# Performance work log

Measured on AMD Instinct MI355X. Metric: run time of the kernel, lower is better.

The kernel has to match this reference:

```python
import jax, jax.numpy as jnp
import numpy as np

WIN = 4096   # win_size == nfft
HOP = 2048   # hop_size == win_size // 2 (COLA)


def _hann_periodic(n):
    # torch.hann_window default is periodic
    return (0.5 * (1.0 - jnp.cos(2.0 * jnp.pi * jnp.arange(n) / n))).astype(jnp.float32)


def _stft(x):
    # x: [B, L] real. Pad to multiple of HOP (as in get_stft_torch), then
    # frame with center=False, apply periodic Hann, one-sided rfft.
    L = x.shape[-1]
    pad = (-L) % HOP
    x = jnp.pad(x, ((0, 0), (0, pad)))
    Lp = L + pad
    T = 1 + (Lp - WIN) // HOP  # number of frames, static
    idx = jnp.arange(T)[:, None] * HOP + jnp.arange(WIN)[None, :]
    frames = x[:, idx] * _hann_periodic(WIN)
    S = jnp.fft.rfft(frames, axis=-1)
    return jnp.swapaxes(S, -1, -2)  # [B, F, T]


def _edr_db(S):
    # Energy decay relief: suffix sum of |S|^2 over time, in dB.
    # Replaces the original O(T^2) per-frame loop with a reverse cumsum.
    p = (S.real * S.real + S.imag * S.imag).astype(jnp.float32)  # [B, F, T]
    suffix = jnp.cumsum(p[..., ::-1], axis=-1)[..., ::-1]
    return 10.0 * jnp.log10(suffix)  # db(x, is_squared=True)


def setup_inputs() -> dict:
    key = jax.random.key(0)
    k1, k2 = jax.random.split(key)
    B, NFREQ = 32, 192000
    return {
        "target_response": jax.random.normal(k1, (B, NFREQ), dtype=jnp.float32),
        "achieved_response": jax.random.normal(k2, (B, NFREQ), dtype=jnp.float32),
    }


def reference(target_response, achieved_response):
    n = target_response.shape[-1]
    # torch.fft.irfft(x, n=x.shape[-1]) -> time-domain RIR of length n
    target_rir = jnp.fft.irfft(target_response, n=n).astype(jnp.float32)
    achieved_rir = jnp.fft.irfft(achieved_response, n=n).astype(jnp.float32)

    S_target = _stft(target_rir)   # [B, F, T] complex64
    S_ach = _stft(achieved_rir)

    target_edr = _edr_db(S_target)  # [B, F, T] float32
    ach_edr = _edr_db(S_ach)

    freq_loss = jnp.sum(jnp.abs(target_edr - ach_edr), axis=-1)  # [B, F]
    loss_per_item = jnp.sum(freq_loss, axis=-1) / jnp.sum(
        jnp.abs(target_edr), axis=(-2, -1)
    )  # [B]
    return jnp.sum(loss_per_item)
```

## Files before the change

### kernel.cpp

```cpp
#include <hip/hip_runtime.h>
#include <hip/hip_fp16.h>
#include <math.h>

#define NSIG 64
#define NROW 192000
#define NN   192000
#define LP   192512
#define NT   93
#define NF   2049
#define PSTR 2050
#define PTS  (NT*PSTR)
#define NK2  188
#define TWO_PI 6.28318530717958647692f
#define SQ2H  0.70710678118654752440f
#define DB_LOG2 3.01029995663981195f

#define WS_P_OFF   0
#define WS_A_OFF   24403200ULL
#define WS_Y_OFF   49044736ULL
#define WS_ACC_OFF 73686272ULL

__device__ __forceinline__ float2 cmul(float2 a, float2 b) {
    return make_float2(a.x*b.x - a.y*b.y, a.x*b.y + a.y*b.x);
}
__device__ __forceinline__ float2 cadd(float2 a, float2 b) {
    return make_float2(a.x + b.x, a.y + b.y);
}
__device__ __forceinline__ float2 csub(float2 a, float2 b) {
    return make_float2(a.x - b.x, a.y - b.y);
}
__device__ __forceinline__ float2 mul_nI(float2 z) { return make_float2(z.y, -z.x); }
__device__ __forceinline__ float2 mul_pI(float2 z) { return make_float2(-z.y, z.x); }
__device__ __forceinline__ __half2 f2h(float2 v) { return __float22half2_rn(v); }
__device__ __forceinline__ float2 h2f(__half2 h) { return __half22float2(h); }

__device__ __forceinline__ void dft8(float2 (&x)[8]) {
    float2 e0 = cadd(x[0], x[4]), e1 = csub(x[0], x[4]);
    float2 e2 = cadd(x[2], x[6]), e3 = csub(x[2], x[6]);
    float2 E0 = cadd(e0, e2), E2 = csub(e0, e2);
    float2 E1 = cadd(e1, mul_nI(e3)), E3 = csub(e1, mul_nI(e3));
    float2 o0 = cadd(x[1], x[5]), o1 = csub(x[1], x[5]);
    float2 o2 = cadd(x[3], x[7]), o3 = csub(x[3], x[7]);
    float2 O0 = cadd(o0, o2), O2 = csub(o0, o2);
    float2 O1 = cadd(o1, mul_nI(o3)), O3 = csub(o1, mul_nI(o3));
    float2 W1 = make_float2(SQ2H*(O1.x + O1.y), SQ2H*(O1.y - O1.x));
    float2 W2 = mul_nI(O2);
    float2 W3 = make_float2(SQ2H*(O3.y - O3.x), -SQ2H*(O3.x + O3.y));
    x[0] = cadd(E0, O0); x[4] = csub(E0, O0);
    x[1] = cadd(E1, W1); x[5] = csub(E1, W1);
    x[2] = cadd(E2, W2); x[6] = csub(E2, W2);
    x[3] = cadd(E3, W3); x[7] = csub(E3, W3);
}

__device__ __forceinline__ void dft8i(float2 (&x)[8]) {
    float2 e0 = cadd(x[0], x[4]), e1 = csub(x[0], x[4]);
    float2 e2 = cadd(x[2], x[6]), e3 = csub(x[2], x[6]);
    float2 E0 = cadd(e0, e2), E2 = csub(e0, e2);
    float2 E1 = cadd(e1, mul_pI(e3)), E3 = csub(e1, mul_pI(e3));
    float2 o0 = cadd(x[1], x[5]), o1 = csub(x[1], x[5]);
    float2 o2 = cadd(x[3], x[7]), o3 = csub(x[3], x[7]);
    float2 O0 = cadd(o0, o2), O2 = csub(o0, o2);
    float2 O1 = cadd(o1, mul_pI(o3)), O3 = csub(o1, mul_pI(o3));
    float2 W1 = make_float2(SQ2H*(O1.x - O1.y), SQ2H*(O1.x + O1.y));
    float2 W2 = mul_pI(O2);
    float2 W3 = make_float2(-SQ2H*(O3.x + O3.y), SQ2H*(O3.x - O3.y));
    x[0] = cadd(E0, O0); x[4] = csub(E0, O0);
    x[1] = cadd(E1, W1); x[5] = csub(E1, W1);
    x[2] = cadd(E2, W2); x[6] = csub(E2, W2);
    x[3] = cadd(E3, W3); x[7] = csub(E3, W3);
}

#define S3C 0.86602540378443865f
__device__ __forceinline__ void dft3i(float2& x0, float2& x1, float2& x2) {
    float2 u = cadd(x1, x2), v = csub(x1, x2);
    float2 w = make_float2(x0.x - 0.5f*u.x, x0.y - 0.5f*u.y);
    x0 = cadd(x0, u);
    float2 iv = make_float2(-S3C * v.y, S3C * v.x);
    x1 = cadd(w, iv);
    x2 = csub(w, iv);
}

#define C51 0.30901699437494742f
#define S51 0.95105651629515357f
#define C52 (-0.80901699437494742f)
#define S52 0.58778525229247313f
__device__ __forceinline__ void dft5i(float2& x0, float2& x1, float2& x2,
                                      float2& x3, float2& x4) {
    float2 t1 = cadd(x1, x4), t2 = csub(x1, x4);
    float2 t3 = cadd(x2, x3), t4 = csub(x2, x3);
    float2 s0 = x0;
    x0 = make_float2(s0.x + t1.x + t3.x, s0.y + t1.y + t3.y);
    float2 A1 = make_float2(s0.x + C51*t1.x + C52*t3.x, s0.y + C51*t1.y + C52*t3.y);
    float2 B1 = make_float2(S51*t2.x + S52*t4.x, S51*t2.y + S52*t4.y);
    float2 A2 = make_float2(s0.x + C52*t1.x + C51*t3.x, s0.y + C52*t1.y + C51*t3.y);
    float2 B2 = make_float2(S52*t2.x - S51*t4.x, S52*t2.y - S51*t4.y);
    x1 = make_float2(A1.x - B1.y, A1.y + B1.x);
    x4 = make_float2(A1.x + B1.y, A1.y - B1.x);
    x2 = make_float2(A2.x - B2.y, A2.y + B2.x);
    x3 = make_float2(A2.x + B2.y, A2.y - B2.x);
}

#define SSTR 520
__global__ void __launch_bounds__(256) k_stage1(const float* __restrict__ X0,
                                                const float* __restrict__ X1,
                                                __half2* __restrict__ A) {
    const int bid  = blockIdx.x;
    const int sig  = bid & 63;
    const int kb   = bid >> 6;
    const int base = kb * 16;
    const float* X = (sig < 32) ? (X0 + (size_t)sig * NROW)
                                : (X1 + (size_t)(sig - 32) * NROW);
    __shared__ float SR[8 * SSTR], SI[8 * SSTR];
    const int tid = threadIdx.x;
    const int row = tid & 7;
    const int ln  = tid >> 3;

    const int k2e0 = base + 2 * row;
    const int k2e  = (k2e0 < NK2) ? k2e0 : (NK2 - 1);
    const int k2o  = (k2e0 + 1 < NK2) ? (k2e0 + 1) : (NK2 - 1);

    #pragma unroll
    for (int m = 0; m < 16; ++m) {
        int i = ln + 32 * m;
        int ide = 375 * i + k2e;
        int ido = 375 * i + k2o;
        float xe = X[(ide <= 96000) ? ide : (NN - ide)];
        float xo = X[(ido <= 96000) ? ido : (NN - ido)];
        SR[SSTR * row + i] = xe;
        SI[SSTR * row + i] = xo;
    }
    __syncthreads();

    const int w = tid >> 6;
    const int l = tid & 63;
    float* sra = SR + SSTR * (2 * w);     float* sia = SI + SSTR * (2 * w);
    float* srb = SR + SSTR * (2 * w + 1); float* sib = SI + SSTR * (2 * w + 1);
    float2 xa[8], xb[8];

    #pragma unroll
    for (int n1 = 0; n1 < 8; ++n1) {
        int ad = l + 64 * n1;
        xa[n1] = make_float2(sra[ad], sia[ad]);
        xb[n1] = make_float2(srb[ad], sib[ad]);
    }
    dft8i(xa); dft8i(xb);
    {
        float sn, cs; __sincosf(TWO_PI * (float)l * (1.0f / 512.0f), &sn, &cs);
        float2 bw = make_float2(cs, sn), tw = bw;
        xa[1] = cmul(xa[1], tw); xb[1] = cmul(xb[1], tw);
        #pragma unroll
        for (int k = 2; k < 8; ++k) {
            tw = cmul(tw, bw);
            xa[k] = cmul(xa[k], tw); xb[k] = cmul(xb[k], tw);
        }
    }
    #pragma unroll
    for (int a2 = 0; a2 < 8; ++a2) {
        int ad = 64 * a2 + (l ^ (8 * a2));
        sra[ad] = xa[a2].x; sia[ad] = xa[a2].y;
        srb[ad] = xb[a2].x; sib[ad] = xb[a2].y;
    }
    __builtin_amdgcn_wave_barrier();

    const int l0 = l & 7, aa = l >> 3;
    #pragma unroll
    for (int l1 = 0; l1 < 8; ++l1) {
        int ad = 64 * aa + ((l0 + 8 * l1) ^ (8 * aa));
        xa[l1] = make_float2(sra[ad], sia[ad]);
        xb[l1] = make_float2(srb[ad], sib[ad]);
    }
    dft8i(xa); dft8i(xb);
    {
        float sn, cs; __sincosf(TWO_PI * (float)l0 * (1.0f / 64.0f), &sn, &cs);
        float2 bw = make_float2(cs, sn), tw = bw;
        xa[1] = cmul(xa[1], tw); xb[1] = cmul(xb[1], tw);
        #pragma unroll
        for (int k = 2; k < 8; ++k) {
            tw = cmul(tw, bw);
            xa[k] = cmul(xa[k], tw); xb[k] = cmul(xb[k], tw);
        }
    }
    #pragma unroll
    for (int b2 = 0; b2 < 8; ++b2) {
        int ad = 64 * b2 + 8 * aa + (l0 ^ b2);
        sra[ad] = xa[b2].x; sia[ad] = xa[b2].y;
        srb[ad] = xb[b2].x; sib[ad] = xb[b2].y;
    }
    __builtin_amdgcn_wave_barrier();

    const int a3 = l & 7, b3 = l >> 3;
    #pragma unroll
    for (int l0r = 0; l0r < 8; ++l0r) {
        int ad = 64 * b3 + 8 * a3 + (l0r ^ b3);
        xa[l0r] = make_float2(sra[ad], sia[ad]);
        xb[l0r] = make_float2(srb[ad], sib[ad]);
    }
    dft8i(xa); dft8i(xb);
    #pragma unroll
    for (int c = 0; c < 8; ++c) {
        int ad = a3 + 8 * b3 + 64 * c;
        sra[ad] = xa[c].x; sia[ad] = xa[c].y;
        srb[ad] = xb[c].x; sib[ad] = xb[c].y;
    }
    __syncthreads();

    if (k2e0 < NK2) {
        float sn, cs;
        __sincosf(TWO_PI * (float)(k2e * ln) * (1.0f / 192000.0f), &sn, &cs);
        float2 wke = make_float2(cs, sn);
        __sincosf(TWO_PI * (float)(32 * k2e) * (1.0f / 192000.0f), &sn, &cs);
        float2 ste = make_float2(cs, sn);
        __sincosf(TWO_PI * (float)(k2o * ln) * (1.0f / 192000.0f), &sn, &cs);
        float2 wko = make_float2(cs, sn);
        __sincosf(TWO_PI * (float)(32 * k2o) * (1.0f / 192000.0f), &sn, &cs);
        float2 sto = make_float2(cs, sn);
        const bool odd_ok = (k2e0 + 1 < NK2);
        __half2* Ae = A + ((size_t)sig * NK2 + k2e) * 512;
        __half2* Ao = A + ((size_t)sig * NK2 + k2o) * 512;
        const float* zr = SR + SSTR * row;
        const float* zi = SI + SSTR * row;
        #pragma unroll
        for (int m = 0; m < 16; ++m) {
            int k  = ln + 32 * m;
            int km = (512 - k) & 511;
            float2 Z  = make_float2(zr[k],  zi[k]);
            float2 Zm = make_float2(zr[km], zi[km]);
            float2 S = make_float2(Z.x + Zm.x, Z.y - Zm.y);
            float2 D = make_float2(Z.x - Zm.x, Z.y + Zm.y);
            float2 Xe = make_float2(0.5f * S.x, 0.5f * S.y);
            float2 Xo = make_float2(0.5f * D.y, -0.5f * D.x);
            Ae[k] = f2h(cmul(Xe, wke));
            if (odd_ok) Ao[k] = f2h(cmul(Xo, wko));
            wke = cmul(wke, ste);
            wko = cmul(wko, sto);
        }
    }
}

#define TP2 16
#define T1STR 17
__global__ void __launch_bounds__(256) k_stage2(const __half2* __restrict__ A,
                                                __half* __restrict__ Y) {
    const int t1b = blockIdx.x * (2 * TP2);
    const int sig = blockIdx.y;
    __shared__ float SRT[375 * T1STR], SIT[375 * T1STR];
    const int tid = threadIdx.x;

    if (blockIdx.x == 0) {
        for (int j = tid; j < 512; j += 256)
            Y[(size_t)sig * LP + NN + j] = __float2half(0.f);
    }

    for (int w = tid; w < 25 * TP2; w += 256) {
        int c = w >> 4, pl = w & 15;
        float2 v[15];
        const float2* Asf = (const float2*)(A + (size_t)sig * (NK2 * 512) + t1b + 2 * pl);
        #pragma unroll
        for (int a = 0; a < 15; ++a) {
            int k2 = 25 * a + c;
            if (k2 < NK2) {
                float2 raw = Asf[(size_t)k2 * 256];
                float2 fa = h2f(((const __half2*)&raw)[0]);
                float2 fb = h2f(((const __half2*)&raw)[1]);
                v[a] = make_float2(fa.x - fb.y, fa.y + fb.x);
            } else {
                float2 raw = Asf[(size_t)(375 - k2) * 256];
                float2 fa = h2f(((const __half2*)&raw)[0]);
                float2 fb = h2f(((const __half2*)&raw)[1]);
                v[a] = make_float2(fa.x + fb.y, fb.x - fa.y);
            }
        }
        #pragma unroll
        for (int r = 0; r < 5; ++r) dft3i(v[r], v[r + 5], v[r + 10]);
        float2 tw[15];
        tw[0] = make_float2(1.f, 0.f);
        float sn, cs; __sincosf(TWO_PI * (float)c * (1.0f / 375.0f), &sn, &cs);
        float2 stp = make_float2(cs, sn);
        #pragma unroll
        for (int e = 1; e < 15; ++e) tw[e] = cmul(tw[e - 1], stp);
        #pragma unroll
        for (int e3 = 0; e3 < 3; ++e3) {
            float2 h0 = v[5 * e3], h1, h2, h3, h4;
            if (e3 == 0) { h1 = v[1]; h2 = v[2]; h3 = v[3]; h4 = v[4]; }
            else if (e3 == 1) {
                h1 = cmul(v[6],  make_float2(0.91354545764260090f, 0.40673664307580021f));
                h2 = cmul(v[7],  make_float2(0.66913060635885821f, 0.74314482547739424f));
                h3 = cmul(v[8],  make_float2(0.30901699437494742f, 0.95105651629515357f));
                h4 = cmul(v[9],  make_float2(-0.10452846326765347f, 0.99452189536827334f));
            } else {
                h1 = cmul(v[11], make_float2(0.66913060635885821f, 0.74314482547739424f));
                h2 = cmul(v[12], make_float2(-0.10452846326765347f, 0.99452189536827334f));
                h3 = cmul(v[13], make_float2(-0.80901699437494742f, 0.58778525229247313f));
                h4 = cmul(v[14], make_float2(-0.97814760073380564f, -0.20791169081775934f));
            }
            dft5i(h0, h1, h2, h3, h4);
            float2 o0 = cmul(h0, tw[e3]);
            float2 o1 = cmul(h1, tw[e3 + 3]);
            float2 o2 = cmul(h2, tw[e3 + 6]);
            float2 o3 = cmul(h3, tw[e3 + 9]);
            float2 o4 = cmul(h4, tw[e3 + 12]);
            int r0 = ((e3     ) * 25 + c) * T1STR + pl;
            int r1 = ((e3 + 3 ) * 25 + c) * T1STR + pl;
            int r2 = ((e3 + 6 ) * 25 + c) * T1STR + pl;
            int r3 = ((e3 + 9 ) * 25 + c) * T1STR + pl;
            int r4 = ((e3 + 12) * 25 + c) * T1STR + pl;
            SRT[r0] = o0.x; SIT[r0] = o0.y;
            SRT[r1] = o1.x; SIT[r1] = o1.y;
            SRT[r2] = o2.x; SIT[r2] = o2.y;
            SRT[r3] = o3.x; SIT[r3] = o3.y;
            SRT[r4] = o4.x; SIT[r4] = o4.y;
        }
    }
    __syncthreads();

    if (tid < 15 * TP2) {
        int e = tid >> 4, pl = tid & 15;
        float2 t[25];
        #pragma unroll
        for (int c = 0; c < 25; ++c) {
            int rr = (e * 25 + c) * T1STR + pl;
            t[c] = make_float2(SRT[rr], SIT[rr]);
        }
        #pragma unroll
        for (int c2 = 0; c2 < 5; ++c2)
            dft5i(t[c2], t[c2 + 5], t[c2 + 10], t[c2 + 15], t[c2 + 20]);
        t[6]  = cmul(t[6],  make_float2(0.96858316112863108f, 0.24868988716485479f));
        t[11] = cmul(t[11], make_float2(0.87630668004386358f, 0.48175367410171532f));
        t[16] = cmul(t[16], make_float2(0.72896862742141155f, 0.68454710592868873f));
        t[21] = cmul(t[21], make_float2(0.53582679497899666f, 0.84432792550201508f));
        t[7]  = cmul(t[7],  make_float2(0.87630668004386358f, 0.48175367410171532f));
        t[12] = cmul(t[12], make_float2(0.53582679497899666f, 0.84432792550201508f));
        t[17] = cmul(t[17], make_float2(0.06279051952931337f, 0.99802672842827156f));
        t[22] = cmul(t[22], make_float2(-0.42577929156507272f, 0.90482705246601958f));
        t[8]  = cmul(t[8],  make_float2(0.72896862742141155f, 0.68454710592868873f));
        t[13] = cmul(t[13], make_float2(0.06279051952931337f, 0.99802672842827156f));
        t[18] = cmul(t[18], make_float2(-0.63742398974868975f, 0.77051324277578925f));
        t[23] = cmul(t[23], make_float2(-0.99211470131447788f, 0.12533323356430426f));
        t[9]  = cmul(t[9],  make_float2(0.53582679497899666f, 0.84432792550201508f));
        t[14] = cmul(t[14], make_float2(-0.42577929156507272f, 0.90482705246601958f));
        t[19] = cmul(t[19], make_float2(-0.99211470131447788f, 0.12533323356430426f));
        t[24] = cmul(t[24], make_float2(-0.63742398974868997f, -0.77051324277578903f));
        #pragma unroll
        for (int u5 = 0; u5 < 5; ++u5)
            dft5i(t[5*u5], t[5*u5 + 1], t[5*u5 + 2], t[5*u5 + 3], t[5*u5 + 4]);
        __half2* yb2 = (__half2*)(Y + (size_t)sig * LP + t1b + 2 * pl);
        #pragma unroll
        for (int u5 = 0; u5 < 5; ++u5)
            #pragma unroll
            for (int u5p = 0; u5p < 5; ++u5p) {
                int d = u5 + 5 * u5p;
                float2 wv = t[5 * u5 + u5p];
                yb2[(size_t)256 * (15 * d + e)] =
                    __floats2half2_rn(wv.x * (1.0f / 192000.0f),
                                      wv.y * (1.0f / 192000.0f));
            }
    }
}

__global__ void __launch_bounds__(256) k_stft(const __half* __restrict__ Y,
                                              __half* __restrict__ P,
                                              float* __restrict__ ACC) {
    const int bid = blockIdx.x;
    const int sig = bid & 63;
    const int fr  = bid >> 6;
    const int lt  = threadIdx.x;
    __shared__ float SR[2560], SI[2560];
    __shared__ float2 wt2[32];
    float2 x[8];
    float2 base2048;

    if (bid == 0 && lt < 64) ACC[lt] = 0.f;

    {
        const __half2* yb = (const __half2*)(Y + (size_t)sig * LP + (size_t)fr * 2048);
        float sn, cs;
        __sincosf(TWO_PI * (float)lt * (1.0f / 2048.0f), &sn, &cs);
        base2048 = make_float2(cs, sn);
        float2 ce = base2048;
        const float2 d1 = make_float2(0.99999882345170188f,
                                      0.00153398018628477f);
        float2 co = cmul(ce, d1);
        const float2 r45 = make_float2(SQ2H, SQ2H);
        #pragma unroll
        for (int r = 0; r < 8; ++r) {
            float2 v = h2f(yb[lt + 256 * r]);
            float we = 0.5f - 0.5f * ce.x;
            float wo = 0.5f - 0.5f * co.x;
            x[r] = make_float2(v.x * we, v.y * wo);
            ce = cmul(ce, r45);
            co = cmul(co, r45);
        }
    }
    dft8(x);
    {
        float2 b = make_float2(base2048.x, -base2048.y), tw = b;
        x[1] = cmul(x[1], tw);
        #pragma unroll
        for (int k = 2; k < 8; ++k) { tw = cmul(tw, b); x[k] = cmul(x[k], tw); }
    }
    #pragma unroll
    for (int k = 0; k < 8; ++k) { SR[k * 256 + lt] = x[k].x; SI[k * 256 + lt] = x[k].y; }
    if (lt < 32) {
        float sn, cs; __sincosf(-TWO_PI * (float)lt * (1.0f / 256.0f), &sn, &cs);
        wt2[lt] = make_float2(cs, sn);
    }
    __syncthreads();

    {
        const int k2 = lt >> 5, m1 = lt & 31;
        #pragma unroll
        for (int r = 0; r < 8; ++r) {
            int idx = k2 * 256 + m1 + 32 * r;
            x[r] = make_float2(SR[idx], SI[idx]);
        }
        dft8(x);
        float2 b = wt2[m1], tw = b;
        x[1] = cmul(x[1], tw);
        #pragma unroll
        for (int k = 2; k < 8; ++k) { tw = cmul(tw, b); x[k] = cmul(x[k], tw); }
        __syncthreads();
        #pragma unroll
        for (int j = 0; j < 8; ++j) {
            int idx = k2 * 288 + j * 36 + m1;
            SR[idx] = x[j].x; SI[idx] = x[j].y;
        }
    }
    __syncthreads();

    {
        const int k2 = lt >> 5, j2 = (lt >> 2) & 7, p1 = lt & 3;
        #pragma unroll
        for (int r = 0; r < 8; ++r) {
            int idx = k2 * 288 + j2 * 36 + p1 + 4 * r;
            x[r] = make_float2(SR[idx], SI[idx]);
        }
        dft8(x);
        float2 b = (p1 == 0) ? make_float2(1.f, 0.f)
                 : (p1 == 1) ? make_float2(0.98078528040323044f, -0.19509032201612827f)
                 : (p1 == 2) ? make_float2(0.92387953251128676f, -0.38268343236508977f)
                 :             make_float2(0.83146961230254524f, -0.55557023301960222f);
        float2 tw = b;
        x[1] = cmul(x[1], tw);
        #pragma unroll
        for (int k = 2; k < 8; ++k) { tw = cmul(tw, b); x[k] = cmul(x[k], tw); }
        __syncthreads();
        #pragma unroll
        for (int q = 0; q < 8; ++q) {
            int idx = 5 * (q * 64 + k2 * 8 + j2) + p1;
            SR[idx] = x[q].x; SI[idx] = x[q].y;
        }
    }
    __syncthreads();

    {
        float2 za[4], zb[4];
        #pragma unroll
        for (int p = 0; p < 4; ++p) {
            int ia = 5 * lt + p;
            za[p] = make_float2(SR[ia], SI[ia]);
            zb[p] = make_float2(SR[ia + 1280], SI[ia + 1280]);
        }
        __syncthreads();
        const int q2a = lt >> 6, k2 = (lt >> 3) & 7, j2 = lt & 7;
        const int kbase = k2 + 8 * j2;
        {
            float2 s0 = cadd(za[0], za[2]), s1 = csub(za[0], za[2]);
            float2 s2 = cadd(za[1], za[3]), s3 = csub(za[1], za[3]);
            float2 X0 = cadd(s0, s2), X2 = csub(s0, s2);
            float2 X1 = cadd(s1, mul_nI(s3)), X3 = csub(s1, mul_nI(s3));
            int ka = kbase + 64 * q2a;
            SR[ka]        = X0.x; SI[ka]        = X0.y;
            SR[ka + 512]  = X1.x; SI[ka + 512]  = X1.y;
            SR[ka + 1024] = X2.x; SI[ka + 1024] = X2.y;
            SR[ka + 1536] = X3.x; SI[ka + 1536] = X3.y;
        }
        {
            float2 s0 = cadd(zb[0], zb[2]), s1 = csub(zb[0], zb[2]);
            float2 s2 = cadd(zb[1], zb[3]), s3 = csub(zb[1], zb[3]);
            float2 X0 = cadd(s0, s2), X2 = csub(s0, s2);
            float2 X1 = cadd(s1, mul_nI(s3)), X3 = csub(s1, mul_nI(s3));
            int kb = kbase + 64 * (q2a + 4);
            SR[kb]        = X0.x; SI[kb]        = X0.y;
            SR[kb + 512]  = X1.x; SI[kb + 512]  = X1.y;
            SR[kb + 1024] = X2.x; SI[kb + 1024] = X2.y;
            SR[kb + 1536] = X3.x; SI[kb + 1536] = X3.y;
        }
    }
    __syncthreads();

    {
        __half* pb = P + (size_t)sig * PTS + (size_t)fr * PSTR;
        float c2 = sqrtf(0.5f * (1.f + base2048.x));
        float s2 = sqrtf(0.5f * (1.f - base2048.x));
        float2 wk = make_float2(c2, -s2);
        const float2 stp = make_float2(0.92387953251128676f,
                                       -0.38268343236508977f);
        #pragma unroll
        for (int j = 0; j < 8; ++j) {
            int k  = lt + 256 * j;
            int kc = (2048 - k) & 2047;
            float zr = SR[k],  zi = SI[k];
            float cr = SR[kc], ci = SI[kc];
            float Ex = 0.5f * (zr + cr), Ey = 0.5f * (zi - ci);
            float Ox = 0.5f * (zi + ci), Oy = -0.5f * (zr - cr);
            float Xx = Ex + wk.x * Ox - wk.y * Oy;
            float Xy = Ey + wk.x * Oy + wk.y * Ox;
            pb[k] = __float2half_rn(sqrtf(Xx * Xx + Xy * Xy));
            wk = cmul(wk, stp);
        }
        if (lt == 0) { float d0 = SR[0] - SI[0]; pb[2048] = __float2half_rn(fabsf(d0)); }
    }
}

__global__ void __launch_bounds__(256) k_edr(const __half* __restrict__ P,
                                             float* __restrict__ ACC) {
    const int b = blockIdx.y;
    const int f = blockIdx.x * 256 + threadIdx.x;
    const bool act = (f < NF);
    const __half* Pt = P + (size_t)b * PTS;
    const __half* Pa = P + (size_t)(b + 32) * PTS;
    float st = 0.f, sa = 0.f, num = 0.f, den = 0.f;
    if (act) {
        for (int t = NT - 1; t >= 0; --t) {
            float vt = __half2float(Pt[(size_t)t * PSTR + f]);
            float va = __half2float(Pa[(size_t)t * PSTR + f]);
            st += vt * vt;
            sa += va * va;
            float et = DB_LOG2 * __log2f(st);
            float ea = DB_LOG2 * __log2f(sa);
            num += fabsf(et - ea);
            den += fabsf(et);
        }
    }
    for (int off = 32; off > 0; off >>= 1) {
        num += __shfl_down(num, off);
        den += __shfl_down(den, off);
    }
    __shared__ float sn_[4], sd_[4];
    int wave = threadIdx.x >> 6, lane = threadIdx.x & 63;
    if (lane == 0) { sn_[wave] = num; sd_[wave] = den; }
    __syncthreads();
    if (threadIdx.x == 0) {
        float n = sn_[0] + sn_[1] + sn_[2] + sn_[3];
        float d = sd_[0] + sd_[1] + sd_[2] + sd_[3];
        atomicAdd(&ACC[2 * b], n);
        atomicAdd(&ACC[2 * b + 1], d);
    }
}

__global__ void k_final(const float* __restrict__ ACC, float* __restrict__ out) {
    int tid = threadIdx.x;
    float r = 0.f;
    if (tid < 32) r = ACC[2 * tid] / ACC[2 * tid + 1];
    for (int off = 32; off > 0; off >>= 1) r += __shfl_down(r, off);
    if (tid == 0) out[0] = r;
}

extern "C" void kernel_launch(void* const* d_in, const int* in_sizes, int n_in,
                              void* d_out, int out_size, void* d_ws, size_t ws_size,
                              hipStream_t stream) {
    const float* X0 = (const float*)d_in[0];
    const float* X1 = (const float*)d_in[1];
    float* out = (float*)d_out;

    char* base = (char*)d_ws;
    __half*  P  = (__half*)(base + WS_P_OFF);
    __half2* A  = (__half2*)(base + WS_A_OFF);
    __half*  Y  = (__half*)(base + WS_Y_OFF);
    float*   ACC = (float*)(base + WS_ACC_OFF);

    k_stage1<<<dim3(768),      dim3(256), 0, stream>>>(X0, X1, A);
    k_stage2<<<dim3(16, 64),   dim3(256), 0, stream>>>(A, Y);
    k_stft  <<<dim3(5952),     dim3(256), 0, stream>>>(Y, P, ACC);
    k_edr   <<<dim3(9, 32),    dim3(256), 0, stream>>>(P, ACC);
    k_final <<<1, 64, 0, stream>>>(ACC, out);
}
```

Before: 79.20 us.

## Give each wave one FFT row in stage1 and double the block count

Stage1 now has each 64-lane wave load and transform a single 512-point row pair (k2e/k2o) on its own, instead of two per wave over a block-shared staging layout. The two block-wide __syncthreads are replaced by wave barriers, shared memory per block is halved, and the grid grows from 768 to 1536 blocks. The aim is more parallelism and occupancy with less block-level synchronisation. Each thread now does half as many FFT rows, which lowers per-thread ILP, and twiddle setup is repeated across twice as many blocks.

```diff
diff --git a/kernel.cpp b/kernel.cpp
--- a/kernel.cpp
+++ b/kernel.cpp
@@ -107,58 +107,50 @@
     const int bid  = blockIdx.x;
     const int sig  = bid & 63;
     const int kb   = bid >> 6;
-    const int base = kb * 16;
+    const int base = kb * 8;
     const float* X = (sig < 32) ? (X0 + (size_t)sig * NROW)
                                 : (X1 + (size_t)(sig - 32) * NROW);
-    __shared__ float SR[8 * SSTR], SI[8 * SSTR];
+    __shared__ float SR[4 * SSTR], SI[4 * SSTR];
     const int tid = threadIdx.x;
-    const int row = tid & 7;
-    const int ln  = tid >> 3;
-
-    const int k2e0 = base + 2 * row;
+    const int w   = tid >> 6;
+    const int l   = tid & 63;
+
+    const int k2e0 = base + 2 * w;
     const int k2e  = (k2e0 < NK2) ? k2e0 : (NK2 - 1);
     const int k2o  = (k2e0 + 1 < NK2) ? (k2e0 + 1) : (NK2 - 1);
 
-    #pragma unroll
-    for (int m = 0; m < 16; ++m) {
-        int i = ln + 32 * m;
+    float* srw = SR + SSTR * w;
+    float* siw = SI + SSTR * w;
+
+    #pragma unroll
+    for (int m = 0; m < 8; ++m) {
+        int i = l + 64 * m;
         int ide = 375 * i + k2e;
         int ido = 375 * i + k2o;
-        float xe = X[(ide <= 96000) ? ide : (NN - ide)];
-        float xo = X[(ido <= 96000) ? ido : (NN - ido)];
-        SR[SSTR * row + i] = xe;
-        SI[SSTR * row + i] = xo;
-    }
-    __syncthreads();
-
-    const int w = tid >> 6;
-    const int l = tid & 63;
-    float* sra = SR + SSTR * (2 * w);     float* sia = SI + SSTR * (2 * w);
-    float* srb = SR + SSTR * (2 * w + 1); float* sib = SI + SSTR * (2 * w + 1);
-    float2 xa[8], xb[8];
+        srw[i] = X[(ide <= 96000) ? ide : (NN - ide)];
+        siw[i] = X[(ido <= 96000) ? ido : (NN - ido)];
+    }
+    __builtin_amdgcn_wave_barrier();
+
+    float2 x[8];
 
     #pragma unroll
     for (int n1 = 0; n1 < 8; ++n1) {
         int ad = l + 64 * n1;
-        xa[n1] = make_float2(sra[ad], sia[ad]);
-        xb[n1] = make_float2(srb[ad], sib[ad]);
-    }
-    dft8i(xa); dft8i(xb);
+        x[n1] = make_float2(srw[ad], siw[ad]);
+    }
+    dft8i(x);
     {
         float sn, cs; __sincosf(TWO_PI * (float)l * (1.0f / 512.0f), &sn, &cs);
         float2 bw = make_float2(cs, sn), tw = bw;
-        xa[1] = cmul(xa[1], tw); xb[1] = cmul(xb[1], tw);
-        #pragma unroll
-        for (int k = 2; k < 8; ++k) {
-            tw = cmul(tw, bw);
-            xa[k] = cmul(xa[k], tw); xb[k] = cmul(xb[k], tw);
-        }
+        x[1] = cmul(x[1], tw);
+        #pragma unroll
+        for (int k = 2; k < 8; ++k) { tw = cmul(tw, bw); x[k] = cmul(x[k], tw); }
     }
     #pragma unroll
     for (int a2 = 0; a2 < 8; ++a2) {
         int ad = 64 * a2 + (l ^ (8 * a2));
-        sra[ad] = xa[a2].x; sia[ad] = xa[a2].y;
-        srb[ad] = xb[a2].x; sib[ad] = xb[a2].y;
+        srw[ad] = x[a2].x; siw[ad] = x[a2].y;
     }
     __builtin_amdgcn_wave_barrier();
 
@@ -166,25 +158,20 @@
     #pragma unroll
     for (int l1 = 0; l1 < 8; ++l1) {
         int ad = 64 * aa + ((l0 + 8 * l1) ^ (8 * aa));
-        xa[l1] = make_float2(sra[ad], sia[ad]);
-        xb[l1] = make_float2(srb[ad], sib[ad]);
-    }
-    dft8i(xa); dft8i(xb);
+        x[l1] = make_float2(srw[ad], siw[ad]);
+    }
+    dft8i(x);
     {
         float sn, cs; __sincosf(TWO_PI * (float)l0 * (1.0f / 64.0f), &sn, &cs);
         float2 bw = make_float2(cs, sn), tw = bw;
-        xa[1] = cmul(xa[1], tw); xb[1] = cmul(xb[1], tw);
-        #pragma unroll
-        for (int k = 2; k < 8; ++k) {
-            tw = cmul(tw, bw);
-            xa[k] = cmul(xa[k], tw); xb[k] = cmul(xb[k], tw);
-        }
+        x[1] = cmul(x[1], tw);
+        #pragma unroll
+        for (int k = 2; k < 8; ++k) { tw = cmul(tw, bw); x[k] = cmul(x[k], tw); }
     }
     #pragma unroll
     for (int b2 = 0; b2 < 8; ++b2) {
         int ad = 64 * b2 + 8 * aa + (l0 ^ b2);
-        sra[ad] = xa[b2].x; sia[ad] = xa[b2].y;
-        srb[ad] = xb[b2].x; sib[ad] = xb[b2].y;
+        srw[ad] = x[b2].x; siw[ad] = x[b2].y;
     }
     __builtin_amdgcn_wave_barrier();
 
@@ -192,39 +179,35 @@
     #pragma unroll
     for (int l0r = 0; l0r < 8; ++l0r) {
         int ad = 64 * b3 + 8 * a3 + (l0r ^ b3);
-        xa[l0r] = make_float2(sra[ad], sia[ad]);
-        xb[l0r] = make_float2(srb[ad], sib[ad]);
-    }
-    dft8i(xa); dft8i(xb);
+        x[l0r] = make_float2(srw[ad], siw[ad]);
+    }
+    dft8i(x);
     #pragma unroll
     for (int c = 0; c < 8; ++c) {
         int ad = a3 + 8 * b3 + 64 * c;
-        sra[ad] = xa[c].x; sia[ad] = xa[c].y;
-        srb[ad] = xb[c].x; sib[ad] = xb[c].y;
-    }
-    __syncthreads();
+        srw[ad] = x[c].x; siw[ad] = x[c].y;
+    }
+    __builtin_amdgcn_wave_barrier();
 
     if (k2e0 < NK2) {
         float sn, cs;
-        __sincosf(TWO_PI * (float)(k2e * ln) * (1.0f / 192000.0f), &sn, &cs);
+        __sincosf(TWO_PI * (float)(k2e * l) * (1.0f / 192000.0f), &sn, &cs);
         float2 wke = make_float2(cs, sn);
-        __sincosf(TWO_PI * (float)(32 * k2e) * (1.0f / 192000.0f), &sn, &cs);
+        __sincosf(TWO_PI * (float)(64 * k2e) * (1.0f / 192000.0f), &sn, &cs);
         float2 ste = make_float2(cs, sn);
-        __sincosf(TWO_PI * (float)(k2o * ln) * (1.0f / 192000.0f), &sn, &cs);
+        __sincosf(TWO_PI * (float)(k2o * l) * (1.0f / 192000.0f), &sn, &cs);
         float2 wko = make_float2(cs, sn);
-        __sincosf(TWO_PI * (float)(32 * k2o) * (1.0f / 192000.0f), &sn, &cs);
+        __sincosf(TWO_PI * (float)(64 * k2o) * (1.0f / 192000.0f), &sn, &cs);
         float2 sto = make_float2(cs, sn);
         const bool odd_ok = (k2e0 + 1 < NK2);
         __half2* Ae = A + ((size_t)sig * NK2 + k2e) * 512;
         __half2* Ao = A + ((size_t)sig * NK2 + k2o) * 512;
-        const float* zr = SR + SSTR * row;
-        const float* zi = SI + SSTR * row;
-        #pragma unroll
-        for (int m = 0; m < 16; ++m) {
-            int k  = ln + 32 * m;
+        #pragma unroll
+        for (int m = 0; m < 8; ++m) {
+            int k  = l + 64 * m;
             int km = (512 - k) & 511;
-            float2 Z  = make_float2(zr[k],  zi[k]);
-            float2 Zm = make_float2(zr[km], zi[km]);
+            float2 Z  = make_float2(srw[k],  siw[k]);
+            float2 Zm = make_float2(srw[km], siw[km]);
             float2 S = make_float2(Z.x + Zm.x, Z.y - Zm.y);
             float2 D = make_float2(Z.x - Zm.x, Z.y + Zm.y);
             float2 Xe = make_float2(0.5f * S.x, 0.5f * S.y);
@@ -569,7 +552,7 @@
     __half*  Y  = (__half*)(base + WS_Y_OFF);
     float*   ACC = (float*)(base + WS_ACC_OFF);
 
-    k_stage1<<<dim3(768),      dim3(256), 0, stream>>>(X0, X1, A);
+    k_stage1<<<dim3(1536),     dim3(256), 0, stream>>>(X0, X1, A);
     k_stage2<<<dim3(16, 64),   dim3(256), 0, stream>>>(A, Y);
     k_stft  <<<dim3(5952),     dim3(256), 0, stream>>>(Y, P, ACC);
     k_edr   <<<dim3(9, 32),    dim3(256), 0, stream>>>(P, ACC);
```

Result: slower. 83.75 us (+5.7%).
